# Optimization experiments

Measured on AMD Instinct MI355X. Metric: run time of the kernel, lower is better.

Reference implementation:

```python
import jax, jax.numpy as jnp
import numpy as np

N_HEADS = 16
LN_EPS = 1e-5


def _rope(x, sin, cos):
    # Faithful to source: uses x.shape[0] (batch here) as 'length'.
    L = x.shape[0]
    x1, x2 = x[..., ::2], x[..., 1::2]
    c = cos[:L, None, :]  # broadcasts over dim 1 (seq)
    s = sin[:L, None, :]
    return jnp.concatenate([x1 * c - x2 * s, x1 * s + x2 * c], axis=-1)


def _layer_norm(x):
    m = jnp.mean(x, axis=-1, keepdims=True)
    v = jnp.var(x, axis=-1, keepdims=True)
    return (x - m) * jax.lax.rsqrt(v + LN_EPS)


def setup_inputs() -> dict:
    key = jax.random.key(0)
    ks = jax.random.split(key, 8)
    B, S, D = 2, 2048, 2048
    CTX = 2048
    x = jax.random.normal(ks[0], (B, S, D), dtype=jnp.float32)
    scale = 0.02
    Wq = jax.random.normal(ks[1], (D, D), dtype=jnp.float32) * scale
    Wk = jax.random.normal(ks[2], (D, D), dtype=jnp.float32) * scale
    Wv = jax.random.normal(ks[3], (D, D), dtype=jnp.float32) * scale
    W1 = jax.random.normal(ks[4], (D, 4 * D), dtype=jnp.float32) * scale
    b1 = jnp.zeros((4 * D,), dtype=jnp.float32)
    W2 = jax.random.normal(ks[5], (4 * D, D), dtype=jnp.float32) * scale
    b2 = jnp.zeros((D,), dtype=jnp.float32)
    inv_freq = 1.0 / (10000.0 ** (jnp.arange(0, D, 2, dtype=jnp.float32) / D))
    sinusoid = jnp.einsum('i,j->ij', jnp.arange(CTX, dtype=jnp.float32), inv_freq)
    sin = jnp.sin(sinusoid)
    cos = jnp.cos(sinusoid)
    return {"x": x, "Wq": Wq, "Wk": Wk, "Wv": Wv, "W1": W1, "b1": b1,
            "W2": W2, "b2": b2, "sin": sin, "cos": cos, "i": 0}


def reference(x, Wq, Wk, Wv, W1, b1, W2, b2, sin, cos, i):
    B, S, D = x.shape
    H = N_HEADS
    hd = D // H
    q = _rope(x @ Wq, sin, cos)
    k = _rope(x @ Wk, sin, cos)
    v = x @ Wv
    # [B,S,D] -> [B,H,S,hd]
    q = q.reshape(B, S, H, hd).transpose(0, 2, 1, 3)
    k = k.reshape(B, S, H, hd).transpose(0, 2, 1, 3)
    v = v.reshape(B, S, H, hd).transpose(0, 2, 1, 3)
    attn = jnp.einsum('bhqd,bhkd->bhqk', q, k) / jnp.sqrt(jnp.float32(hd))
    causal = jnp.tril(jnp.ones((S, S), dtype=bool))
    attn = jnp.where(causal[None, None], attn, -jnp.inf)
    attn = jax.nn.softmax(attn, axis=-1)
    out = jnp.einsum('bhqk,bhkd->bhqd', attn, v)
    out = out.transpose(0, 2, 1, 3).reshape(B, S, D)
    out = _layer_norm(out + x)
    h = jax.nn.gelu(out @ W1 + b1, approximate=False)
    out2 = _layer_norm(h @ W2 + b2 + out)
    return out2
```

## Files before the change

kernel.cpp:

```cpp
#include <hip/hip_runtime.h>
#include <hip/hip_bf16.h>
#include <math.h>
#include <stdint.h>

using bf16 = __hip_bfloat16;
typedef __attribute__((ext_vector_type(4))) float f32x4;
typedef __attribute__((ext_vector_type(8))) short s16x8;

#define MFMA16(a, b, c) __builtin_amdgcn_mfma_f32_16x16x32_bf16(a, b, c, 0, 0, 0)

__device__ __forceinline__ void gload_lds16(const void* g, void* l) {
    __builtin_amdgcn_global_load_lds(
        (const __attribute__((address_space(1))) void*)g,
        (__attribute__((address_space(3))) void*)l, 16, 0, 0);
}

struct alignas(16) bf16x8s { bf16 v[8]; };

__global__ void cvt_f32_bf16(const float* __restrict__ in, bf16* __restrict__ out, long n) {
    long i = ((long)blockIdx.x * 256 + threadIdx.x) * 8;
    if (i >= n) return;
    float4 a = *(const float4*)(in + i);
    float4 b = *(const float4*)(in + i + 4);
    bf16x8s r;
    r.v[0] = __float2bfloat16(a.x); r.v[1] = __float2bfloat16(a.y);
    r.v[2] = __float2bfloat16(a.z); r.v[3] = __float2bfloat16(a.w);
    r.v[4] = __float2bfloat16(b.x); r.v[5] = __float2bfloat16(b.y);
    r.v[6] = __float2bfloat16(b.z); r.v[7] = __float2bfloat16(b.w);
    *(bf16x8s*)(out + i) = r;
}

__global__ void transpose_cvt(const float* __restrict__ W, bf16* __restrict__ Wt, int K, int N) {
    __shared__ bf16 t[32][33];
    int tx = threadIdx.x & 31, ty = threadIdx.x >> 5;
    int n0 = blockIdx.x * 32, k0 = blockIdx.y * 32;
    #pragma unroll
    for (int r = ty; r < 32; r += 8)
        t[r][tx] = __float2bfloat16(W[(size_t)(k0 + r) * N + n0 + tx]);
    __syncthreads();
    #pragma unroll
    for (int r = ty; r < 32; r += 8)
        Wt[(size_t)(n0 + r) * K + k0 + tx] = t[tx][r];
}

template <int EPI, int SPLITK>
__global__ __launch_bounds__(512) void gemm_pipe(
    const bf16* __restrict__ A, const bf16* __restrict__ Bt,
    void* __restrict__ C, const float* __restrict__ bias,
    const float* __restrict__ resid, int M, int N, int K)
{
    __shared__ __align__(16) char smem[131072];
    const int tid = threadIdx.x;
    const int wid = tid >> 6, lane = tid & 63;
    const int quad = lane >> 4, l16 = lane & 15;
    const int wm = wid >> 2, wn = wid & 3;

    const int nx = gridDim.x;
    const int nwg = nx * gridDim.y;
    int lin = blockIdx.y * nx + blockIdx.x;
    const int cpx = nwg >> 3;
    lin = (lin & 7) * cpx + (lin >> 3);
    const int bm = (lin % nx) * 256, bn = (lin / nx) * 256;

    const int KH = K / SPLITK;
    const int kbeg = blockIdx.z * KH;
    const int NT = KH / 64;

    const int r0 = tid >> 3, pb = tid & 7;
    const int gcol = ((pb ^ (r0 & 7)) << 3);
    const bf16* pA00 = A + (size_t)(bm + r0) * K + kbeg + gcol;
    const bf16* pB00 = Bt + (size_t)(bn + (r0 >> 5) * 64 + (r0 & 31)) * K + kbeg + gcol;
    const int dA = tid * 16;
    const int dB = 32768 + tid * 16;

#define ST_A(h, sb, T1) { \
    gload_lds16(pA00 + (size_t)((h) * 64      ) * K + (T1) * 64, smem + (sb) + (h) * 16384 + dA); \
    gload_lds16(pA00 + (size_t)((h) * 64 + 128) * K + (T1) * 64, smem + (sb) + (h) * 16384 + dA + 8192); }
#define ST_B(h, sb, T1) { \
    gload_lds16(pB00 + (size_t)((h) * 32      ) * K + (T1) * 64, smem + (sb) + (h) * 16384 + dB); \
    gload_lds16(pB00 + (size_t)((h) * 32 + 128) * K + (T1) * 64, smem + (sb) + (h) * 16384 + dB + 8192); }

    const int asw = l16 & 7;
    const int kx0 = (quad ^ asw) << 3;
    const int kx1 = ((4 + quad) ^ asw) << 3;
    const int aq0 = wm * 4096 + l16 * 64;
    const int aq1 = 8192 + wm * 4096 + l16 * 64;
    const int bq0 = 16384 + wn * 2048 + l16 * 64;
    const int bq1 = bq0 + 8192;
    const bf16* sm = (const bf16*)smem;

#define LD_A(dst, off) { _Pragma("unroll") for (int mt = 0; mt < 4; ++mt) { \
    dst[0][mt] = *(const s16x8*)(sm + (off) + mt * 1024 + kx0); \
    dst[1][mt] = *(const s16x8*)(sm + (off) + mt * 1024 + kx1); } }
#define LD_B(dst, off) { _Pragma("unroll") for (int nt = 0; nt < 2; ++nt) { \
    dst[0][nt] = *(const s16x8*)(sm + (off) + nt * 1024 + kx0); \
    dst[1][nt] = *(const s16x8*)(sm + (off) + nt * 1024 + kx1); } }
#define MM(fa, fb, mo, no) { \
    __builtin_amdgcn_s_setprio(1); \
    _Pragma("unroll") for (int kh = 0; kh < 2; ++kh) \
    _Pragma("unroll") for (int mt = 0; mt < 4; ++mt) \
    _Pragma("unroll") for (int nt = 0; nt < 2; ++nt) \
        acc[(mo) + mt][(no) + nt] = MFMA16(fa[kh][mt], fb[kh][nt], acc[(mo) + mt][(no) + nt]); \
    __builtin_amdgcn_s_setprio(0); }

    f32x4 acc[8][4] = {};
    s16x8 fA0[2][4], fA1[2][4], fB0[2][2], fB1[2][2];

    ST_A(0, 0, 0); ST_B(0, 0, 0); ST_A(1, 0, 0);
    ST_B(1, 0, 0);
    asm volatile("s_waitcnt vmcnt(2)\ns_barrier" ::: "memory");
    LD_A(fA0, aq0); LD_B(fB0, bq0);

    for (int t = 0; t < NT - 1; ++t) {
        const int ce = (t & 1) << 15;
        const int ne = ce ^ 32768;
        const int nb = ne << 1;
        LD_A(fA1, ce + aq1);
        ST_A(0, nb, t + 1); ST_B(0, nb, t + 1); ST_A(1, nb, t + 1);
        MM(fA0, fB0, 0, 0);
        asm volatile("s_waitcnt vmcnt(6)\ns_barrier" ::: "memory");
        LD_B(fB1, ce + bq1);
        ST_B(1, nb, t + 1);
        MM(fA1, fB0, 4, 0);
        MM(fA0, fB1, 0, 2);
        asm volatile("s_waitcnt vmcnt(2)\ns_barrier" ::: "memory");
        LD_A(fA0, ne + aq0); LD_B(fB0, ne + bq0);
        MM(fA1, fB1, 4, 2);
    }
    {
        const int ce = ((NT - 1) & 1) << 15;
        LD_A(fA1, ce + aq1);
        MM(fA0, fB0, 0, 0);
        asm volatile("s_waitcnt vmcnt(0)\ns_barrier" ::: "memory");
        LD_B(fB1, ce + bq1);
        MM(fA1, fB0, 4, 0);
        MM(fA0, fB1, 0, 2);
        MM(fA1, fB1, 4, 2);
    }
#undef ST_A
#undef ST_B
#undef LD_A
#undef LD_B
#undef MM

    float* Cp = (float*)C;
    if (EPI == 3) Cp += (size_t)blockIdx.z * M * N;

    #pragma unroll
    for (int m = 0; m < 8; ++m) {
        #pragma unroll
        for (int n = 0; n < 4; ++n) {
            #pragma unroll
            for (int r = 0; r < 4; ++r) {
                int row = bm + wm * 128 + m * 16 + quad * 4 + r;
                int col = bn + wn * 64 + n * 16 + l16;
                float v = acc[m][n][r];
                if (EPI == 0) {
                    ((bf16*)C)[(size_t)row * N + col] = __float2bfloat16(v);
                } else if (EPI == 1) {
                    float xx = v + bias[col];
                    float g = 0.5f * xx * (1.0f + erff(xx * 0.7071067811865475f));
                    ((bf16*)C)[(size_t)row * N + col] = __float2bfloat16(g);
                } else if (EPI == 2) {
                    ((float*)C)[(size_t)row * N + col] =
                        v + bias[col] + resid[(size_t)row * N + col];
                } else {
                    Cp[(size_t)row * N + col] = v;
                }
            }
        }
    }
}

__global__ void rope_kernel(const bf16* __restrict__ in, bf16* __restrict__ out,
                            const float* __restrict__ sn, const float* __restrict__ cs,
                            int S, int D, int instride) {
    int row = blockIdx.x;
    int pos = row / S;
    const int half = D >> 1;
    const bf16* r = in + (size_t)row * instride;
    bf16* o = out + (size_t)row * D;
    for (int j = threadIdx.x; j < half; j += 256) {
        uint32_t pr = *(const uint32_t*)(r + 2 * j);
        float x1 = __uint_as_float(pr << 16);
        float x2 = __uint_as_float(pr & 0xffff0000u);
        float c = cs[(size_t)pos * half + j], s = sn[(size_t)pos * half + j];
        o[j]        = __float2bfloat16(x1 * c - x2 * s);
        o[half + j] = __float2bfloat16(x1 * s + x2 * c);
    }
}

__global__ void vtrans_kernel(const bf16* __restrict__ v, bf16* __restrict__ vt,
                              int S, int D, int H, int instride) {
    __shared__ bf16 t[32][33];
    int bh = blockIdx.z, b = bh >> 4, h = bh & 15;
    int s0 = blockIdx.x * 32, d0 = blockIdx.y * 32;
    int tx = threadIdx.x & 31, ty = threadIdx.x >> 5;
    #pragma unroll
    for (int r = ty; r < 32; r += 8)
        t[r][tx] = v[(size_t)(b * S + s0 + r) * instride + h * 128 + d0 + tx];
    __syncthreads();
    #pragma unroll
    for (int r = ty; r < 32; r += 8)
        vt[((size_t)bh * 128 + d0 + r) * S + s0 + tx] = t[tx][r];
}

__global__ __launch_bounds__(256, 4) void attn_kernel(
    const bf16* __restrict__ q, const bf16* __restrict__ k, const bf16* __restrict__ vt,
    float* __restrict__ o, int S, int D, int H)
{
    __shared__ __align__(16) char smem[40960];
    bf16* Ks = (bf16*)smem;
    bf16* Vs = (bf16*)(smem + 16384);
    bf16* Ps = (bf16*)(smem + 32768);

    const int tid = threadIdx.x, wid = tid >> 6, lane = tid & 63;
    const int quad = lane >> 4, l16 = lane & 15;
    const int bh = blockIdx.x, b = bh >> 4, h = bh & 15;
    const int qt = gridDim.y - 1 - blockIdx.y;
    const float scale = 0.08838834764831845f;

    s16x8 qf[4];
    const bf16* qrow = q + ((size_t)(b * S + qt * 64 + wid * 16 + l16)) * D + h * 128;
    #pragma unroll
    for (int ks = 0; ks < 4; ++ks)
        qf[ks] = *(const s16x8*)(qrow + ks * 32 + quad * 8);

    f32x4 oacc[8] = {};
    float mstate = -INFINITY, lstate = 0.f;

    const bf16* kb0 = k + (size_t)(b * S) * D + h * 128;
    const bf16* vb0 = vt + (size_t)bh * 128 * S;
    bf16* psw = Ps + wid * 16 * 64;
    const int sw = l16 & 7;
    const int nch = qt + 1;

    for (int kc = 0; kc < nch; ++kc) {
        __syncthreads();
        #pragma unroll
        for (int c = 0; c < 4; ++c) {
            int choff = (wid * 4 + c) << 10;
            int off = choff + lane * 16;
            int rk = off >> 8, bk = (off & 255) >> 4;
            gload_lds16(kb0 + (size_t)(kc * 64 + rk) * D + ((bk ^ (rk & 7)) << 3),
                        (char*)Ks + choff);
            int rv = off >> 7, bv = (off & 127) >> 4;
            gload_lds16(vb0 + (size_t)rv * S + kc * 64 + ((bv ^ (rv & 7)) << 3),
                        (char*)Vs + choff);
        }
        __syncthreads();

        f32x4 sacc[4] = {};
        #pragma unroll
        for (int mt = 0; mt < 4; ++mt) {
            #pragma unroll
            for (int ks = 0; ks < 4; ++ks) {
                s16x8 kf = *(const s16x8*)(Ks + (mt * 16 + l16) * 128 +
                                           (((ks * 4 + quad) ^ sw) << 3));
                sacc[mt] = MFMA16(kf, qf[ks], sacc[mt]);
            }
        }

        const bool need_mask = (kc == qt);
        #pragma unroll
        for (int mt = 0; mt < 4; ++mt)
            #pragma unroll
            for (int r = 0; r < 4; ++r) {
                float vv = sacc[mt][r] * scale;
                if (need_mask) {
                    int kl = mt * 16 + quad * 4 + r;
                    if (kl > wid * 16 + l16) vv = -INFINITY;
                }
                sacc[mt][r] = vv;
            }

        float mx = fmaxf(fmaxf(fmaxf(sacc[0][0], sacc[0][1]), fmaxf(sacc[0][2], sacc[0][3])),
                         fmaxf(fmaxf(sacc[1][0], sacc[1][1]), fmaxf(sacc[1][2], sacc[1][3])));
        mx = fmaxf(mx, fmaxf(fmaxf(fmaxf(sacc[2][0], sacc[2][1]), fmaxf(sacc[2][2], sacc[2][3])),
                             fmaxf(fmaxf(sacc[3][0], sacc[3][1]), fmaxf(sacc[3][2], sacc[3][3]))));
        mx = fmaxf(mx, __shfl_xor(mx, 16, 64));
        mx = fmaxf(mx, __shfl_xor(mx, 32, 64));
        float mnew = fmaxf(mstate, mx);
        float alpha = __expf(mstate - mnew);
        float rs = 0.f;
        #pragma unroll
        for (int mt = 0; mt < 4; ++mt)
            #pragma unroll
            for (int r = 0; r < 4; ++r) {
                float p = __expf(sacc[mt][r] - mnew);
                sacc[mt][r] = p;
                rs += p;
            }
        rs += __shfl_xor(rs, 16, 64);
        rs += __shfl_xor(rs, 32, 64);
        lstate = lstate * alpha + rs;
        mstate = mnew;
        #pragma unroll
        for (int mt = 0; mt < 8; ++mt)
            #pragma unroll
            for (int r = 0; r < 4; ++r) oacc[mt][r] *= alpha;

        #pragma unroll
        for (int mt = 0; mt < 4; ++mt)
            #pragma unroll
            for (int r = 0; r < 4; ++r) {
                int kl = mt * 16 + quad * 4 + r;
                psw[l16 * 64 + (((kl >> 3) ^ sw) << 3) + (kl & 7)] =
                    __float2bfloat16(sacc[mt][r]);
            }

        #pragma unroll
        for (int ks2 = 0; ks2 < 2; ++ks2) {
            s16x8 pf = *(const s16x8*)(psw + l16 * 64 + (((ks2 * 4 + quad) ^ sw) << 3));
            #pragma unroll
            for (int mt = 0; mt < 8; ++mt) {
                s16x8 vf = *(const s16x8*)(Vs + (mt * 16 + l16) * 64 +
                                           (((ks2 * 4 + quad) ^ sw) << 3));
                oacc[mt] = MFMA16(vf, pf, oacc[mt]);
            }
        }
    }

    float inv = 1.0f / lstate;
    __syncthreads();
    float* osw = (float*)smem + wid * 16 * 130;
    #pragma unroll
    for (int mt = 0; mt < 8; ++mt)
        #pragma unroll
        for (int r = 0; r < 4; ++r)
            osw[l16 * 130 + mt * 16 + quad * 4 + r] = oacc[mt][r] * inv;
    float* obase = o + (size_t)(b * S + qt * 64 + wid * 16) * D + h * 128;
    #pragma unroll
    for (int r16 = 0; r16 < 16; ++r16) {
        float2 val = *(const float2*)(osw + r16 * 130 + lane * 2);
        *(float2*)(obase + (size_t)r16 * D + lane * 2) = val;
    }
}

__global__ __launch_bounds__(256) void ln_kernel(
    const float* __restrict__ a, const float* __restrict__ b,
    const float* __restrict__ c, const float* __restrict__ bias,
    float* __restrict__ outf, bf16* __restrict__ outb, int D)
{
    int row = blockIdx.x;
    const float* pa = a + (size_t)row * D;
    const float* pb = b ? b + (size_t)row * D : nullptr;
    const float* pc = c ? c + (size_t)row * D : nullptr;
    float v[8];
    float sum = 0.f, sq = 0.f;
    #pragma unroll
    for (int u = 0; u < 8; ++u) {
        int j = threadIdx.x + u * 256;
        float x = pa[j];
        if (pb) x += pb[j];
        if (pc) x += pc[j];
        if (bias) x += bias[j];
        v[u] = x; sum += x; sq += x * x;
    }
    #pragma unroll
    for (int off = 32; off > 0; off >>= 1) {
        sum += __shfl_down(sum, off, 64);
        sq  += __shfl_down(sq,  off, 64);
    }
    __shared__ float red[8];
    int wid = threadIdx.x >> 6, lane = threadIdx.x & 63;
    if (lane == 0) { red[wid] = sum; red[4 + wid] = sq; }
    __syncthreads();
    sum = red[0] + red[1] + red[2] + red[3];
    sq  = red[4] + red[5] + red[6] + red[7];
    float mean = sum / D;
    float var = sq / D - mean * mean;
    float rstd = rsqrtf(fmaxf(var, 0.f) + 1e-5f);
    float* pof = outf ? outf + (size_t)row * D : nullptr;
    bf16* pob = outb ? outb + (size_t)row * D : nullptr;
    #pragma unroll
    for (int u = 0; u < 8; ++u) {
        int j = threadIdx.x + u * 256;
        float y = (v[u] - mean) * rstd;
        if (pof) pof[j] = y;
        if (pob) pob[j] = __float2bfloat16(y);
    }
}

extern "C" void kernel_launch(void* const* d_in, const int* in_sizes, int n_in,
                              void* d_out, int out_size, void* d_ws, size_t ws_size,
                              hipStream_t stream) {
    const float* x  = (const float*)d_in[0];
    const float* Wq = (const float*)d_in[1];
    const float* Wk = (const float*)d_in[2];
    const float* Wv = (const float*)d_in[3];
    const float* W1 = (const float*)d_in[4];
    const float* b1 = (const float*)d_in[5];
    const float* W2 = (const float*)d_in[6];
    const float* b2 = (const float*)d_in[7];
    const float* sn = (const float*)d_in[8];
    const float* cs = (const float*)d_in[9];

    const int B = 2, S = 2048, D = 2048, H = 16, Dff = 8192;
    const int M = B * S;
    const int NQKV = 3 * D;
    char* ws = (char*)d_ws;
    const size_t MB = 1024 * 1024;

    const size_t o_xb   = 0;
    const size_t o_Wqkv = 16 * MB;
    const size_t o_qkv  = 40 * MB;
    const size_t o_qr   = 0;
    const size_t o_kr   = 16 * MB;
    const size_t o_vt   = 88 * MB;
    const size_t o_attn = 40 * MB;
    const size_t o_outb = 0;
    const size_t o_outf = 72 * MB;
    const size_t o_W1t  = 16 * MB;
    const size_t o_h    = 104 * MB;
    const size_t o_W2t  = 16 * MB;
    const size_t o_p    = 168 * MB;

    long nx = (long)M * D;
    cvt_f32_bf16<<<nx / 2048, 256, 0, stream>>>(x, (bf16*)(ws + o_xb), nx);
    transpose_cvt<<<dim3(D / 32, D / 32), 256, 0, stream>>>(
        Wq, (bf16*)(ws + o_Wqkv), D, D);
    transpose_cvt<<<dim3(D / 32, D / 32), 256, 0, stream>>>(
        Wk, (bf16*)(ws + o_Wqkv) + (size_t)D * D, D, D);
    transpose_cvt<<<dim3(D / 32, D / 32), 256, 0, stream>>>(
        Wv, (bf16*)(ws + o_Wqkv) + 2 * (size_t)D * D, D, D);

    gemm_pipe<0, 1><<<dim3(M / 256, NQKV / 256), 512, 0, stream>>>(
        (bf16*)(ws + o_xb), (bf16*)(ws + o_Wqkv), ws + o_qkv, nullptr, nullptr,
        M, NQKV, D);

    rope_kernel<<<M, 256, 0, stream>>>((bf16*)(ws + o_qkv), (bf16*)(ws + o_qr),
                                       sn, cs, S, D, NQKV);
    rope_kernel<<<M, 256, 0, stream>>>((bf16*)(ws + o_qkv) + D, (bf16*)(ws + o_kr),
                                       sn, cs, S, D, NQKV);
    vtrans_kernel<<<dim3(S / 32, 4, B * H), 256, 0, stream>>>(
        (bf16*)(ws + o_qkv) + 2 * D, (bf16*)(ws + o_vt), S, D, H, NQKV);

    attn_kernel<<<dim3(B * H, S / 64), 256, 0, stream>>>(
        (bf16*)(ws + o_qr), (bf16*)(ws + o_kr), (bf16*)(ws + o_vt),
        (float*)(ws + o_attn), S, D, H);

    ln_kernel<<<M, 256, 0, stream>>>((float*)(ws + o_attn), x, nullptr, nullptr,
                                     (float*)(ws + o_outf), (bf16*)(ws + o_outb), D);

    transpose_cvt<<<dim3(Dff / 32, D / 32), 256, 0, stream>>>(
        W1, (bf16*)(ws + o_W1t), D, Dff);
    gemm_pipe<1, 1><<<dim3(M / 256, Dff / 256), 512, 0, stream>>>(
        (bf16*)(ws + o_outb), (bf16*)(ws + o_W1t), ws + o_h, b1, nullptr, M, Dff, D);

    transpose_cvt<<<dim3(D / 32, Dff / 32), 256, 0, stream>>>(
        W2, (bf16*)(ws + o_W2t), Dff, D);
    gemm_pipe<3, 2><<<dim3(M / 256, D / 256, 2), 512, 0, stream>>>(
        (bf16*)(ws + o_h), (bf16*)(ws + o_W2t), ws + o_p, nullptr, nullptr, M, D, Dff);

    ln_kernel<<<M, 256, 0, stream>>>((float*)(ws + o_p),
                                     (float*)(ws + o_p) + (size_t)M * D,
                                     (float*)(ws + o_outf), b2,
                                     (float*)d_out, nullptr, D);
}
```

Before: 797.6 us.

## Restructure GEMM main loop into 8-phase ping-pong schedule with finer-grained prefetch

Replaces the two-stage GEMM main loop with an unrolled-by-two, eight-phase schedule. Each phase loads one A or B fragment from LDS, issues one quarter of the next tile's global-to-LDS copies, and runs one quarter of the MFMAs, with explicit barriers and lgkmcnt waits around each phase. This is meant to interleave memory traffic with matrix math more evenly and to cut register use by keeping a single A fragment buffer. In exchange it adds many more barriers per K-step, and it assumes NT is even.

```diff
diff --git a/kernel.cpp b/kernel.cpp
--- a/kernel.cpp
+++ b/kernel.cpp
@@ -84,7 +84,7 @@
     const int kx0 = (quad ^ asw) << 3;
     const int kx1 = ((4 + quad) ^ asw) << 3;
     const int aq0 = wm * 4096 + l16 * 64;
-    const int aq1 = 8192 + wm * 4096 + l16 * 64;
+    const int aq1 = 8192 + aq0;
     const int bq0 = 16384 + wn * 2048 + l16 * 64;
     const int bq1 = bq0 + 8192;
     const bf16* sm = (const bf16*)smem;
@@ -102,46 +102,73 @@
     _Pragma("unroll") for (int nt = 0; nt < 2; ++nt) \
         acc[(mo) + mt][(no) + nt] = MFMA16(fa[kh][mt], fb[kh][nt], acc[(mo) + mt][(no) + nt]); \
     __builtin_amdgcn_s_setprio(0); }
+#define BARM  asm volatile("s_barrier" ::: "memory")
+#define LGKM0 asm volatile("s_waitcnt lgkmcnt(0)" ::: "memory")
 
     f32x4 acc[8][4] = {};
-    s16x8 fA0[2][4], fA1[2][4], fB0[2][2], fB1[2][2];
-
-    ST_A(0, 0, 0); ST_B(0, 0, 0); ST_A(1, 0, 0);
-    ST_B(1, 0, 0);
-    asm volatile("s_waitcnt vmcnt(2)\ns_barrier" ::: "memory");
-    LD_A(fA0, aq0); LD_B(fB0, bq0);
-
-    for (int t = 0; t < NT - 1; ++t) {
-        const int ce = (t & 1) << 15;
-        const int ne = ce ^ 32768;
-        const int nb = ne << 1;
-        LD_A(fA1, ce + aq1);
-        ST_A(0, nb, t + 1); ST_B(0, nb, t + 1); ST_A(1, nb, t + 1);
-        MM(fA0, fB0, 0, 0);
-        asm volatile("s_waitcnt vmcnt(6)\ns_barrier" ::: "memory");
-        LD_B(fB1, ce + bq1);
-        ST_B(1, nb, t + 1);
-        MM(fA1, fB0, 4, 0);
-        MM(fA0, fB1, 0, 2);
-        asm volatile("s_waitcnt vmcnt(2)\ns_barrier" ::: "memory");
-        LD_A(fA0, ne + aq0); LD_B(fB0, ne + bq0);
-        MM(fA1, fB1, 4, 2);
+    s16x8 fA[2][4], fBa[2][2], fBb[2][2];
+
+    ST_A(0, 0, 0); ST_B(1, 0, 0); ST_A(1, 0, 0); ST_B(0, 0, 0);
+    ST_A(0, 65536, 1); ST_B(1, 65536, 1); ST_A(1, 65536, 1);
+    asm volatile("s_waitcnt vmcnt(6)" ::: "memory");
+    BARM;
+
+    for (int it = 0; it < NT / 2 - 1; ++it) {
+        const int T = 2 * it;
+        LD_A(fA, aq0); LD_B(fBa, bq0);
+        ST_B(0, 65536, T + 1);
+        BARM; LGKM0; MM(fA, fBa, 0, 0); BARM;
+        LD_B(fBb, bq1);
+        ST_A(0, 0, T + 2);
+        BARM; LGKM0; MM(fA, fBb, 0, 2); BARM;
+        LD_A(fA, aq1);
+        ST_B(1, 0, T + 2);
+        BARM; LGKM0; MM(fA, fBb, 4, 2); BARM;
+        LD_B(fBa, bq0);
+        ST_A(1, 0, T + 2);
+        asm volatile("s_waitcnt vmcnt(6)" ::: "memory");
+        BARM; LGKM0; MM(fA, fBa, 4, 0); BARM;
+        LD_A(fA, 32768 + aq0); LD_B(fBa, 32768 + bq0);
+        ST_B(0, 0, T + 2);
+        BARM; LGKM0; MM(fA, fBa, 0, 0); BARM;
+        LD_B(fBb, 32768 + bq1);
+        ST_A(0, 65536, T + 3);
+        BARM; LGKM0; MM(fA, fBb, 0, 2); BARM;
+        LD_A(fA, 32768 + aq1);
+        ST_B(1, 65536, T + 3);
+        BARM; LGKM0; MM(fA, fBb, 4, 2); BARM;
+        LD_B(fBa, 32768 + bq0);
+        ST_A(1, 65536, T + 3);
+        asm volatile("s_waitcnt vmcnt(6)" ::: "memory");
+        BARM; LGKM0; MM(fA, fBa, 4, 0); BARM;
     }
     {
-        const int ce = ((NT - 1) & 1) << 15;
-        LD_A(fA1, ce + aq1);
-        MM(fA0, fB0, 0, 0);
-        asm volatile("s_waitcnt vmcnt(0)\ns_barrier" ::: "memory");
-        LD_B(fB1, ce + bq1);
-        MM(fA1, fB0, 4, 0);
-        MM(fA0, fB1, 0, 2);
-        MM(fA1, fB1, 4, 2);
+        LD_A(fA, aq0); LD_B(fBa, bq0);
+        ST_B(0, 65536, NT - 1);
+        BARM; LGKM0; MM(fA, fBa, 0, 0); BARM;
+        LD_B(fBb, bq1);
+        BARM; LGKM0; MM(fA, fBb, 0, 2); BARM;
+        LD_A(fA, aq1);
+        BARM; LGKM0; MM(fA, fBb, 4, 2); BARM;
+        LD_B(fBa, bq0);
+        asm volatile("s_waitcnt vmcnt(0)" ::: "memory");
+        BARM; LGKM0; MM(fA, fBa, 4, 0); BARM;
+        LD_A(fA, 32768 + aq0); LD_B(fBa, 32768 + bq0);
+        BARM; LGKM0; MM(fA, fBa, 0, 0); BARM;
+        LD_B(fBb, 32768 + bq1);
+        BARM; LGKM0; MM(fA, fBb, 0, 2); BARM;
+        LD_A(fA, 32768 + aq1);
+        BARM; LGKM0; MM(fA, fBb, 4, 2); BARM;
+        LD_B(fBa, 32768 + bq0);
+        LGKM0; MM(fA, fBa, 4, 0);
     }
 #undef ST_A
 #undef ST_B
 #undef LD_A
 #undef LD_B
 #undef MM
+#undef BARM
+#undef LGKM0
 
     float* Cp = (float*)C;
     if (EPI == 3) Cp += (size_t)blockIdx.z * M * N;
```

Measured after the change: 796.2 us. Within noise of the previous version (-0.2%).
